# Optimization experiments

Hardware: AMD Instinct MI355X
Metric: run time of the kernel (lower is better)

Reference implementation:

```python
import jax, jax.numpy as jnp
import numpy as np

J = 4  # number of wavelet scales


def _wavelet(P, X, mask):
    """Graph diffusion wavelet features for one (batch, time) slice.
    P: [N,N] transition matrix, X: [N,F] node features, mask: [N].
    Returns flattened pooled features [K*F], K = 1 + J + J*(J-1)/2.
    """
    P_pow = P
    F1, F2, PSI = [], [], []
    for _ in range(J):
        new_P = P_pow @ P_pow              # P^{2^{i+1}}
        psi = new_P - P_pow                # psi_i = P^{2^{i+1}} - P^{2^i}
        sc = jnp.abs(psi @ X)              # |psi_i X|  [N,F]
        F1.append(sc)
        for prev_psi in PSI:               # second order: |psi_j |psi_i X||, j < i
            F2.append(jnp.abs(prev_psi @ sc))
        PSI.append(psi)
        P_pow = new_P
    F0 = P_pow @ X                         # zeroth order: P^{2^J} X
    feats = jnp.stack([F0, *F1, *F2])      # [K, N, F]
    # pooling: mean over nodes (normalized by mask.sum()), then flatten
    return (feats.sum(axis=1) / mask.sum()).reshape(-1)


def setup_inputs() -> dict:
    key = jax.random.key(0)
    k1, k2 = jax.random.split(key)
    B, T, N, F = 8, 4, 1024, 64
    A = jax.random.uniform(k1, (B, T, N, N), dtype=jnp.float32)
    P = A / A.sum(axis=-1, keepdims=True)  # row-stochastic transition matrix
    X = jax.random.normal(k2, (B, T, N, F), dtype=jnp.float32)
    mask = jnp.ones((B, T, N), dtype=jnp.float32)
    return {"P": P, "X": X, "mask": mask}


def reference(P, X, mask):
    return jax.vmap(jax.vmap(_wavelet))(P, X, mask)  # [B, T, K*F]
```

## Files before the change

kernel.cpp:

```cpp
#include <hip/hip_runtime.h>

typedef unsigned short u16;
typedef __bf16 bfx8 __attribute__((ext_vector_type(8)));
typedef float f32x4 __attribute__((ext_vector_type(4)));
typedef unsigned short u16x4 __attribute__((ext_vector_type(4)));

#define NN 1024
#define FF 64
#define NSLICE 32
#define KFEAT 11

#define POOL_BYTES (NSLICE * KFEAT * FF * 4)
#define MSUM_OFF   POOL_BYTES
#define SLICE0     ((size_t)1 << 20)
#define MB1        (1024u * 1024u)
#define KB128      (131072u)
#define KB256      (262144u)
#define OFF_P    0u
#define OFF_PT   (2u * MB1)
#define OFF_P2   (4u * MB1)
#define OFF_XT   (6u * MB1)
#define OFF_Y2T  (6u * MB1 + 1u * KB128)
#define OFF_Y4T  (6u * MB1 + 2u * KB128)
#define OFF_Y6T  (6u * MB1 + 3u * KB128)
#define OFF_Y8T  (6u * MB1 + 4u * KB128)
#define OFF_Y10T (6u * MB1 + 5u * KB128)
#define OFF_Y12T (6u * MB1 + 6u * KB128)
#define OFF_Y14T (6u * MB1 + 7u * KB128)
#define OFF_S1T  (6u * MB1 + 8u * KB128)
#define OFF_S2T  (6u * MB1 + 9u * KB128)
#define OFF_S3T  (6u * MB1 + 10u * KB128)
#define OFF_TQ2  (6u * MB1 + 11u * KB128)
#define OFF_TQ3  (6u * MB1 + 12u * KB128)
#define OFF_TW4  (6u * MB1 + 13u * KB128)
#define OFF_TP6  (6u * MB1 + 14u * KB128)
#define OFF_Y1   (8u * MB1)
#define OFF_Y2   (8u * MB1 + 1u * KB256)
#define OFF_Y4   (8u * MB1 + 2u * KB256)
#define OFF_Y8   (8u * MB1 + 3u * KB256)
#define OFF_PS1  (8u * MB1 + 4u * KB256)
#define OFF_PS2  (8u * MB1 + 5u * KB256)
#define OFF_PS3  (8u * MB1 + 6u * KB256)
#define OFF_QS2  (8u * MB1 + 7u * KB256)
#define OFF_QS3  (8u * MB1 + 8u * KB256)
#define OFF_W4   (8u * MB1 + 9u * KB256)
#define PS_BYTES ((size_t)(11u * MB1))

#define GL16(g, l) __builtin_amdgcn_global_load_lds( \
    (const __attribute__((address_space(1))) unsigned int*)(g), \
    (__attribute__((address_space(3))) unsigned int*)(l), 16, 0, 0)


__device__ __forceinline__ u16 f2b(float v) {
  __bf16 h = (__bf16)v;
  return __builtin_bit_cast(u16, h);
}

__global__ void k_convP(const float* __restrict__ P, char* ws, int sliceBase) {
  __shared__ float tile[64][65];
  int s = blockIdx.z;
  const float* Ps = P + (size_t)(sliceBase + s) * NN * NN;
  char* base = ws + SLICE0 + (size_t)s * PS_BYTES;
  u16* Pb  = (u16*)(base + OFF_P);
  u16* PbT = (u16*)(base + OFF_PT);
  int r0 = blockIdx.y * 64, c0 = blockIdx.x * 64;
  int tid = threadIdx.x;
  int tc = tid & 15, tr = tid >> 4;
  for (int rr = 0; rr < 64; rr += 16) {
    int r = rr + tr;
    float4 v = *(const float4*)&Ps[(size_t)(r0 + r) * NN + c0 + tc * 4];
    tile[r][tc * 4 + 0] = v.x;
    tile[r][tc * 4 + 1] = v.y;
    tile[r][tc * 4 + 2] = v.z;
    tile[r][tc * 4 + 3] = v.w;
    u16x4 pk = {f2b(v.x), f2b(v.y), f2b(v.z), f2b(v.w)};
    *(u16x4*)&Pb[(size_t)(r0 + r) * NN + c0 + tc * 4] = pk;
  }
  __syncthreads();
  for (int it = 0; it < 4; ++it) {
    int oc = (tid >> 4) + it * 16;
    int ch = tid & 15;
    u16x4 pk = {f2b(tile[ch * 4 + 0][oc]), f2b(tile[ch * 4 + 1][oc]),
                f2b(tile[ch * 4 + 2][oc]), f2b(tile[ch * 4 + 3][oc])};
    *(u16x4*)&PbT[(size_t)(c0 + oc) * NN + r0 + ch * 4] = pk;
  }
}

__global__ void k_convX(const float* __restrict__ X, char* ws, int sliceBase) {
  __shared__ float tile[64][65];
  int s = blockIdx.z;
  const float* Xs = X + (size_t)(sliceBase + s) * NN * FF;
  u16* XT = (u16*)(ws + SLICE0 + (size_t)s * PS_BYTES + OFF_XT);
  int r0 = blockIdx.x * 64;
  int tx = threadIdx.x & 63, ty = threadIdx.x >> 6;
  for (int rr = 0; rr < 64; rr += 4)
    tile[rr + ty][tx] = Xs[(size_t)(r0 + rr + ty) * FF + tx];
  __syncthreads();
  for (int rr = 0; rr < 64; rr += 4)
    XT[(size_t)(rr + ty) * NN + r0 + tx] = f2b(tile[tx][rr + ty]);
}

__global__ void k_msum(const float* __restrict__ mask, float* msum) {
  int s = blockIdx.x;
  const float* m = mask + (size_t)s * NN;
  int t = threadIdx.x;
  float v = m[t] + m[t + 256] + m[t + 512] + m[t + 768];
  for (int o = 32; o; o >>= 1) v += __shfl_down(v, o);
  __shared__ float ps[4];
  if ((t & 63) == 0) ps[t >> 6] = v;
  __syncthreads();
  if (t == 0) msum[s] = ps[0] + ps[1] + ps[2] + ps[3];
}

__global__ __launch_bounds__(256)
void k_square(char* ws) {
  __shared__ u16 sh[16384];

  unsigned nwg = gridDim.x, wg = blockIdx.x;
  unsigned newid = (wg & 7) * (nwg >> 3) + (wg >> 3);
  int z = newid >> 6;
  int by = (newid >> 3) & 7, bx = newid & 7;

  char* base = ws + SLICE0 + (size_t)z * PS_BYTES;
  const u16* A  = (const u16*)(base + OFF_P);
  const u16* Bt = (const u16*)(base + OFF_PT);
  u16* C        = (u16*)(base + OFF_P2);

  const int tid = threadIdx.x;
  const int lane = tid & 63, wave = tid >> 6;
  const int wr = wave >> 1, wc = wave & 1;
  const int l16 = lane & 15, lk = lane >> 4;
  const int bm = by * 128, bn = bx * 128;

  const int pc = (((tid & 3) - (tid >> 3)) & 3) << 3;
  const u16* gA = A + (size_t)(bm + (tid >> 2)) * NN + pc;
  const u16* gB = Bt + (size_t)(bn + (tid >> 2)) * NN + pc;
  const int rot = ((lk + (l16 >> 1)) & 3) << 3;

  f32x4 acc[4][4] = {};

#define SQ_STAGE(k0, buf)                                   \
  {                                                         \
    u16* dA = sh + (buf)*4096 + wave * 512;                 \
    u16* dB = sh + 8192 + (buf)*4096 + wave * 512;          \
    GL16(gA + (k0), dA);                                    \
    GL16(gA + 64 * NN + (k0), dA + 2048);                   \
    GL16(gB + (k0), dB);                                    \
    GL16(gB + 64 * NN + (k0), dB + 2048);                   \
  }

#define SQ_COMPUTE(buf)                                                      \
  {                                                                          \
    const u16* bA = sh + (buf)*4096;                                         \
    const u16* bB = sh + 8192 + (buf)*4096;                                  \
    bfx8 af[4], bf[4];                                                       \
    _Pragma("unroll") for (int m = 0; m < 4; ++m)                            \
        af[m] = *(const bfx8*)&bA[(wr * 64 + m * 16 + l16) * 32 + rot];      \
    _Pragma("unroll") for (int n = 0; n < 4; ++n)                            \
        bf[n] = *(const bfx8*)&bB[(wc * 64 + n * 16 + l16) * 32 + rot];      \
    __builtin_amdgcn_s_setprio(1);                                           \
    _Pragma("unroll") for (int m = 0; m < 4; ++m)                            \
        _Pragma("unroll") for (int n = 0; n < 4; ++n)                        \
            acc[m][n] = __builtin_amdgcn_mfma_f32_16x16x32_bf16(             \
                af[m], bf[n], acc[m][n], 0, 0, 0);                           \
    __builtin_amdgcn_s_setprio(0);                                           \
  }

  SQ_STAGE(0, 0);
#pragma unroll 2
  for (int t = 1; t < 32; ++t) {
    SQ_STAGE(t * 32, t & 1);
    asm volatile("s_waitcnt vmcnt(4)" ::: "memory");
    __builtin_amdgcn_s_barrier();
    SQ_COMPUTE((t - 1) & 1);
    __builtin_amdgcn_s_barrier();
  }
  asm volatile("s_waitcnt vmcnt(0)" ::: "memory");
  __builtin_amdgcn_s_barrier();
  SQ_COMPUTE(1);

#pragma unroll
  for (int m = 0; m < 4; ++m) {
    int row0 = bm + wr * 64 + m * 16 + lk * 4;
#pragma unroll
    for (int n = 0; n < 4; ++n) {
      int col = bn + wc * 64 + n * 16 + l16;
#pragma unroll
      for (int r = 0; r < 4; ++r)
        C[(size_t)(row0 + r) * NN + col] = f2b(acc[m][n][r]);
    }
  }
}

struct NA {
  int a, rawK;
  int bt[3], d[3], pk[3], f[3], ta[3], tv[3];
};

template <int NB>
__global__ __launch_bounds__(256)
void k_nar(char* ws, int sliceBase, float* __restrict__ pooled, NA na) {
  __shared__ u16 sh[16384];
  unsigned nwg = gridDim.x, wg = blockIdx.x;
  unsigned newid = (wg & 7) * (nwg >> 3) + (wg >> 3);
  int by = newid & 15;
  int s = newid >> 4;
  char* base = ws + SLICE0 + (size_t)s * PS_BYTES;

  const u16* A = (const u16*)(base + na.a);
  int poolBase = (sliceBase + s) * (KFEAT * FF);

  const int tid = threadIdx.x;
  const int lane = tid & 63, wave = tid >> 6;
  const int wr = wave >> 1, wc = wave & 1;
  const int l16 = lane & 15, lk = lane >> 4;
  const int bm = by * 64;

  const int pc = (((tid & 3) - (tid >> 3)) & 3) << 3;
  const u16* gA = A + (size_t)(bm + (tid >> 2)) * NN + pc;
  const u16* gB[NB];
#pragma unroll
  for (int j = 0; j < NB; ++j)
    gB[j] = (const u16*)(base + na.bt[j]) + (size_t)(tid >> 2) * NN + pc;
  const int rot = ((lk + (l16 >> 1)) & 3) << 3;

  f32x4 acc[NB][2][2] = {};

  auto STAGE = [&](int k0, int buf) {
    u16* dA = sh + buf * 8192 + wave * 512;
    GL16(gA + k0, dA);
#pragma unroll
    for (int j = 0; j < NB; ++j) {
      u16* dB = sh + buf * 8192 + 2048 + j * 2048 + wave * 512;
      GL16(gB[j] + k0, dB);
    }
  };
  auto COMPUTE = [&](int buf) {
    const u16* bA = sh + buf * 8192;
    bfx8 af[2];
#pragma unroll
    for (int m = 0; m < 2; ++m)
      af[m] = *(const bfx8*)&bA[(wr * 32 + m * 16 + l16) * 32 + rot];
    __builtin_amdgcn_s_setprio(1);
#pragma unroll
    for (int j = 0; j < NB; ++j) {
      const u16* bB = sh + buf * 8192 + 2048 + j * 2048;
      bfx8 bf[2];
#pragma unroll
      for (int n = 0; n < 2; ++n)
        bf[n] = *(const bfx8*)&bB[(wc * 32 + n * 16 + l16) * 32 + rot];
#pragma unroll
      for (int m = 0; m < 2; ++m)
#pragma unroll
        for (int n = 0; n < 2; ++n)
          acc[j][m][n] = __builtin_amdgcn_mfma_f32_16x16x32_bf16(
              af[m], bf[n], acc[j][m][n], 0, 0, 0);
    }
    __builtin_amdgcn_s_setprio(0);
  };

  STAGE(0, 0);
#pragma unroll 2
  for (int t = 1; t < 32; ++t) {
    STAGE(t * 32, t & 1);
    if constexpr (NB == 1)
      asm volatile("s_waitcnt vmcnt(2)" ::: "memory");
    else if constexpr (NB == 2)
      asm volatile("s_waitcnt vmcnt(3)" ::: "memory");
    else
      asm volatile("s_waitcnt vmcnt(4)" ::: "memory");
    __builtin_amdgcn_s_barrier();
    COMPUTE((t - 1) & 1);
    __builtin_amdgcn_s_barrier();
  }
  asm volatile("s_waitcnt vmcnt(0)" ::: "memory");
  __builtin_amdgcn_s_barrier();
  COMPUTE(1);

#pragma unroll
  for (int j = 0; j < NB; ++j) {
    const float* D = na.d[j] >= 0 ? (const float*)(base + na.d[j]) : nullptr;
    float* F  = na.f[j]  >= 0 ? (float*)(base + na.f[j])  : nullptr;
    u16* Ta   = na.ta[j] >= 0 ? (u16*)(base + na.ta[j])   : nullptr;
    u16* Tv   = na.tv[j] >= 0 ? (u16*)(base + na.tv[j])   : nullptr;
    bool doRaw = (j == 0) && (na.rawK >= 0);

    float ps[2] = {0.f, 0.f};
    float pr[2] = {0.f, 0.f};

#pragma unroll
    for (int m = 0; m < 2; ++m) {
      int row0 = bm + wr * 32 + m * 16 + lk * 4;
#pragma unroll
      for (int n = 0; n < 2; ++n) {
        int col = wc * 32 + n * 16 + l16;
        float v0 = acc[j][m][n][0], v1 = acc[j][m][n][1];
        float v2 = acc[j][m][n][2], v3 = acc[j][m][n][3];
        float w0 = v0, w1 = v1, w2 = v2, w3 = v3;
        if (D) {
          w0 = v0 - D[(size_t)(row0 + 0) * FF + col];
          w1 = v1 - D[(size_t)(row0 + 1) * FF + col];
          w2 = v2 - D[(size_t)(row0 + 2) * FF + col];
          w3 = v3 - D[(size_t)(row0 + 3) * FF + col];
        }
        float a0 = fabsf(w0), a1 = fabsf(w1), a2 = fabsf(w2), a3 = fabsf(w3);
        if (na.pk[j] >= 0) ps[n] += a0 + a1 + a2 + a3;
        if (doRaw) pr[n] += v0 + v1 + v2 + v3;
        if (F) {
          F[(size_t)(row0 + 0) * FF + col] = v0;
          F[(size_t)(row0 + 1) * FF + col] = v1;
          F[(size_t)(row0 + 2) * FF + col] = v2;
          F[(size_t)(row0 + 3) * FF + col] = v3;
        }
        if (Ta) {
          u16x4 pkk = {f2b(a0), f2b(a1), f2b(a2), f2b(a3)};
          *(u16x4*)&Ta[(size_t)col * NN + row0] = pkk;
        }
        if (Tv) {
          u16x4 pkk = {f2b(v0), f2b(v1), f2b(v2), f2b(v3)};
          *(u16x4*)&Tv[(size_t)col * NN + row0] = pkk;
        }
      }
    }

    if (na.pk[j] >= 0) {
#pragma unroll
      for (int n = 0; n < 2; ++n) {
        float v = ps[n];
        v += __shfl_xor(v, 16);
        v += __shfl_xor(v, 32);
        if (lane < 16)
          atomicAdd(&pooled[poolBase + na.pk[j] * FF + wc * 32 + n * 16 + lane], v);
      }
    }
    if (doRaw) {
#pragma unroll
      for (int n = 0; n < 2; ++n) {
        float v = pr[n];
        v += __shfl_xor(v, 16);
        v += __shfl_xor(v, 32);
        if (lane < 16)
          atomicAdd(&pooled[poolBase + na.rawK * FF + wc * 32 + n * 16 + lane], v);
      }
    }
  }
}

__global__ void k_final(const float* __restrict__ pooled, const float* __restrict__ msum,
                        float* __restrict__ out, int total) {
  int i = blockIdx.x * 256 + threadIdx.x;
  if (i < total) out[i] = pooled[i] / msum[i / (KFEAT * FF)];
}

static NA mk1(int a, int rawK, int bt, int d, int pk, int f, int ta, int tv) {
  NA x;
  x.a = a; x.rawK = rawK;
  for (int j = 0; j < 3; ++j) {
    x.bt[j] = -1; x.d[j] = -1; x.pk[j] = -1;
    x.f[j] = -1; x.ta[j] = -1; x.tv[j] = -1;
  }
  x.bt[0] = bt; x.d[0] = d; x.pk[0] = pk; x.f[0] = f; x.ta[0] = ta; x.tv[0] = tv;
  return x;
}
static void setslot(NA& x, int j, int bt, int d, int pk, int f, int ta, int tv) {
  x.bt[j] = bt; x.d[j] = d; x.pk[j] = pk; x.f[j] = f; x.ta[j] = ta; x.tv[j] = tv;
}

extern "C" void kernel_launch(void* const* d_in, const int* in_sizes, int n_in,
                              void* d_out, int out_size, void* d_ws, size_t ws_size,
                              hipStream_t stream) {
  const float* P = (const float*)d_in[0];
  const float* X = (const float*)d_in[1];
  const float* mask = (const float*)d_in[2];
  float* out = (float*)d_out;
  char* ws = (char*)d_ws;
  float* pooled = (float*)ws;
  float* msum = (float*)(ws + MSUM_OFF);

  hipMemsetAsync(pooled, 0, POOL_BYTES, stream);
  k_msum<<<NSLICE, 256, 0, stream>>>(mask, msum);

  int S = 1;
  if (ws_size > SLICE0 + PS_BYTES) S = (int)((ws_size - SLICE0) / PS_BYTES);
  if (S > NSLICE) S = NSLICE;
  if (S < 1) S = 1;

  for (int b0 = 0; b0 < NSLICE; b0 += S) {
    int n = (NSLICE - b0 < S) ? (NSLICE - b0) : S;
    k_convP<<<dim3(16, 16, n), 256, 0, stream>>>(P, ws, b0);
    k_convX<<<dim3(16, 1, n), 256, 0, stream>>>(X, ws, b0);
    k_square<<<64 * n, 256, 0, stream>>>(ws);

    NA c1 = mk1(OFF_P, -1, OFF_XT, -1, -1, OFF_Y1, -1, -1);
    k_nar<1><<<16 * n, 256, 0, stream>>>(ws, b0, pooled, c1);
    NA c2 = mk1(OFF_P2, -1, OFF_XT, (int)OFF_Y1, 1, OFF_Y2, -1, OFF_Y2T);
    k_nar<1><<<16 * n, 256, 0, stream>>>(ws, b0, pooled, c2);
    NA c3 = mk1(OFF_P2, -1, OFF_Y2T, (int)OFF_Y2, 2, OFF_Y4, OFF_S1T, OFF_Y4T);
    k_nar<1><<<16 * n, 256, 0, stream>>>(ws, b0, pooled, c3);
    NA c4 = mk1(OFF_P2, -1, OFF_Y4T, -1, -1, -1, -1, OFF_Y6T);
    k_nar<1><<<16 * n, 256, 0, stream>>>(ws, b0, pooled, c4);
    NA c5 = mk1(OFF_P2, -1, OFF_Y6T, (int)OFF_Y4, 3, OFF_Y8, OFF_S2T, OFF_Y8T);
    k_nar<1><<<16 * n, 256, 0, stream>>>(ws, b0, pooled, c5);
    NA c6 = mk1(OFF_P2, -1, OFF_Y8T, -1, -1, -1, -1, OFF_Y10T);
    k_nar<1><<<16 * n, 256, 0, stream>>>(ws, b0, pooled, c6);
    NA c7 = mk1(OFF_P2, -1, OFF_Y10T, -1, -1, -1, -1, OFF_Y12T);
    k_nar<1><<<16 * n, 256, 0, stream>>>(ws, b0, pooled, c7);
    NA c8 = mk1(OFF_P2, -1, OFF_Y12T, -1, -1, -1, -1, OFF_Y14T);
    k_nar<1><<<16 * n, 256, 0, stream>>>(ws, b0, pooled, c8);
    NA c9 = mk1(OFF_P2, 0, OFF_Y14T, (int)OFF_Y8, 4, -1, OFF_S3T, -1);
    k_nar<1><<<16 * n, 256, 0, stream>>>(ws, b0, pooled, c9);

    NA c10 = mk1(OFF_P, -1, OFF_S1T, -1, -1, OFF_PS1, -1, -1);
    setslot(c10, 1, OFF_S2T, -1, -1, OFF_PS2, -1, -1);
    setslot(c10, 2, OFF_S3T, -1, -1, OFF_PS3, -1, -1);
    k_nar<3><<<16 * n, 256, 0, stream>>>(ws, b0, pooled, c10);
    NA c11 = mk1(OFF_P2, -1, OFF_S1T, (int)OFF_PS1, 5, -1, -1, -1);
    setslot(c11, 1, OFF_S2T, (int)OFF_PS2, 6, OFF_QS2, -1, OFF_TQ2);
    setslot(c11, 2, OFF_S3T, (int)OFF_PS3, 8, OFF_QS3, -1, OFF_TQ3);
    k_nar<3><<<16 * n, 256, 0, stream>>>(ws, b0, pooled, c11);
    NA c12 = mk1(OFF_P2, -1, OFF_TQ2, (int)OFF_QS2, 7, -1, -1, -1);
    setslot(c12, 1, OFF_TQ3, (int)OFF_QS3, 9, OFF_W4, -1, OFF_TW4);
    k_nar<2><<<16 * n, 256, 0, stream>>>(ws, b0, pooled, c12);
    NA c13 = mk1(OFF_P2, -1, OFF_TW4, -1, -1, -1, -1, OFF_TP6);
    k_nar<1><<<16 * n, 256, 0, stream>>>(ws, b0, pooled, c13);
    NA c14 = mk1(OFF_P2, -1, OFF_TP6, (int)OFF_W4, 10, -1, -1, -1);
    k_nar<1><<<16 * n, 256, 0, stream>>>(ws, b0, pooled, c14);
  }
  int total = NSLICE * KFEAT * FF;
  k_final<<<(total + 255) / 256, 256, 0, stream>>>(pooled, msum, out, total);
}
```

Measured before the change: 392.0 us.

## Load MFMA operands directly from global memory, dropping LDS double-buffering in k_nar

The narrow GEMM kernel no longer stages A and B tiles through shared memory with async global-to-LDS loads, barriers and double buffering. Each lane now reads its bf16 fragments straight from global memory into registers in a fully unrolled K loop. This removes LDS traffic, barrier stalls and waitcnt bookkeeping, but each wave now fetches its data independently, so operands shared across waves are read redundantly and latency hiding depends on the compiler scheduling loads ahead.

```diff
diff --git a/kernel.cpp b/kernel.cpp
--- a/kernel.cpp
+++ b/kernel.cpp
@@ -50,7 +50,6 @@
     (const __attribute__((address_space(1))) unsigned int*)(g), \
     (__attribute__((address_space(3))) unsigned int*)(l), 16, 0, 0)
 
-
 __device__ __forceinline__ u16 f2b(float v) {
   __bf16 h = (__bf16)v;
   return __builtin_bit_cast(u16, h);
@@ -200,7 +199,6 @@
 template <int NB>
 __global__ __launch_bounds__(256)
 void k_nar(char* ws, int sliceBase, float* __restrict__ pooled, NA na) {
-  __shared__ u16 sh[16384];
   unsigned nwg = gridDim.x, wg = blockIdx.x;
   unsigned newid = (wg & 7) * (nwg >> 3) + (wg >> 3);
   int by = newid & 15;
@@ -216,66 +214,29 @@
   const int l16 = lane & 15, lk = lane >> 4;
   const int bm = by * 64;
 
-  const int pc = (((tid & 3) - (tid >> 3)) & 3) << 3;
-  const u16* gA = A + (size_t)(bm + (tid >> 2)) * NN + pc;
-  const u16* gB[NB];
+  const u16* pA = A + (size_t)(bm + wr * 32 + l16) * NN + lk * 8;
+  const u16* pB[NB];
 #pragma unroll
   for (int j = 0; j < NB; ++j)
-    gB[j] = (const u16*)(base + na.bt[j]) + (size_t)(tid >> 2) * NN + pc;
-  const int rot = ((lk + (l16 >> 1)) & 3) << 3;
+    pB[j] = (const u16*)(base + na.bt[j]) + (size_t)(wc * 32 + l16) * NN + lk * 8;
 
   f32x4 acc[NB][2][2] = {};
 
-  auto STAGE = [&](int k0, int buf) {
-    u16* dA = sh + buf * 8192 + wave * 512;
-    GL16(gA + k0, dA);
+#pragma unroll
+  for (int t = 0; t < 32; ++t) {
+    const int k0 = t * 32;
+    bfx8 a0 = *(const bfx8*)(pA + k0);
+    bfx8 a1 = *(const bfx8*)(pA + 16 * NN + k0);
 #pragma unroll
     for (int j = 0; j < NB; ++j) {
-      u16* dB = sh + buf * 8192 + 2048 + j * 2048 + wave * 512;
-      GL16(gB[j] + k0, dB);
-    }
-  };
-  auto COMPUTE = [&](int buf) {
-    const u16* bA = sh + buf * 8192;
-    bfx8 af[2];
-#pragma unroll
-    for (int m = 0; m < 2; ++m)
-      af[m] = *(const bfx8*)&bA[(wr * 32 + m * 16 + l16) * 32 + rot];
-    __builtin_amdgcn_s_setprio(1);
-#pragma unroll
-    for (int j = 0; j < NB; ++j) {
-      const u16* bB = sh + buf * 8192 + 2048 + j * 2048;
-      bfx8 bf[2];
-#pragma unroll
-      for (int n = 0; n < 2; ++n)
-        bf[n] = *(const bfx8*)&bB[(wc * 32 + n * 16 + l16) * 32 + rot];
-#pragma unroll
-      for (int m = 0; m < 2; ++m)
-#pragma unroll
-        for (int n = 0; n < 2; ++n)
-          acc[j][m][n] = __builtin_amdgcn_mfma_f32_16x16x32_bf16(
-              af[m], bf[n], acc[j][m][n], 0, 0, 0);
-    }
-    __builtin_amdgcn_s_setprio(0);
-  };
-
-  STAGE(0, 0);
-#pragma unroll 2
-  for (int t = 1; t < 32; ++t) {
-    STAGE(t * 32, t & 1);
-    if constexpr (NB == 1)
-      asm volatile("s_waitcnt vmcnt(2)" ::: "memory");
-    else if constexpr (NB == 2)
-      asm volatile("s_waitcnt vmcnt(3)" ::: "memory");
-    else
-      asm volatile("s_waitcnt vmcnt(4)" ::: "memory");
-    __builtin_amdgcn_s_barrier();
-    COMPUTE((t - 1) & 1);
-    __builtin_amdgcn_s_barrier();
-  }
-  asm volatile("s_waitcnt vmcnt(0)" ::: "memory");
-  __builtin_amdgcn_s_barrier();
-  COMPUTE(1);
+      bfx8 b0 = *(const bfx8*)(pB[j] + k0);
+      bfx8 b1 = *(const bfx8*)(pB[j] + 16 * NN + k0);
+      acc[j][0][0] = __builtin_amdgcn_mfma_f32_16x16x32_bf16(a0, b0, acc[j][0][0], 0, 0, 0);
+      acc[j][0][1] = __builtin_amdgcn_mfma_f32_16x16x32_bf16(a0, b1, acc[j][0][1], 0, 0, 0);
+      acc[j][1][0] = __builtin_amdgcn_mfma_f32_16x16x32_bf16(a1, b0, acc[j][1][0], 0, 0, 0);
+      acc[j][1][1] = __builtin_amdgcn_mfma_f32_16x16x32_bf16(a1, b1, acc[j][1][1], 0, 0, 0);
+    }
+  }
 
 #pragma unroll
   for (int j = 0; j < NB; ++j) {
```

New measurement: 682.9 us. 1.74x slower.
